# Kernel tuning notes

Measured on AMD Instinct MI355X. Metric: run time of the kernel, lower is better.

Reference implementation:

```python
import jax, jax.numpy as jnp
import numpy as np

B, S = 128, 400
EMB, ENC, DEC = 128, 1024, 300
VOCAB, MAX_OOV = 50000, 50


def setup_inputs() -> dict:
    key = jax.random.key(0)
    ks = jax.random.split(key, 16)
    s = 0.05
    return {
        "embedded": jax.random.normal(ks[0], (B, EMB), jnp.float32),
        "enc_output": jax.random.normal(ks[1], (B, S, ENC), jnp.float32),
        "h1": jax.random.normal(ks[2], (B, DEC), jnp.float32),
        "pad_mask": jnp.zeros((B, S), jnp.bool_),
        "max_n_oov": MAX_OOV,
        "source_WORD_encoding_extended": jax.random.randint(ks[3], (B, S), 0, VOCAB + MAX_OOV),
        # parameters
        "W_attn1": jax.random.normal(ks[4], (ENC, DEC), jnp.float32) * s,
        "W_attn2": jax.random.normal(ks[5], (ENC, DEC), jnp.float32) * s,
        "W_ih": jax.random.normal(ks[6], (3 * DEC, EMB + ENC), jnp.float32) * s,
        "W_hh": jax.random.normal(ks[7], (3 * DEC, DEC), jnp.float32) * s,
        "b_ih": jax.random.normal(ks[8], (3 * DEC,), jnp.float32) * s,
        "b_hh": jax.random.normal(ks[9], (3 * DEC,), jnp.float32) * s,
        "W_out": jax.random.normal(ks[10], (VOCAB, ENC + DEC), jnp.float32) * s,
        "b_out": jax.random.normal(ks[11], (VOCAB,), jnp.float32) * s,
        "W_p": jax.random.normal(ks[12], (1, ENC + DEC), jnp.float32) * s,
        "b_p": jax.random.normal(ks[13], (1,), jnp.float32) * s,
    }


def _additive_attn(h, enc_output, W, pad_mask):
    # h: [B, DEC], enc_output: [B, S, ENC], W: [ENC, DEC]
    e = jnp.einsum('bse,ed->bsd', enc_output, W)
    scores = jnp.einsum('bd,bsd->bs', h, e)
    scores = jnp.where(pad_mask, -jnp.inf, scores)
    return jax.nn.softmax(scores, axis=1)  # [B, S]


def _gru_cell(x, h, W_ih, W_hh, b_ih, b_hh):
    gx = x @ W_ih.T + b_ih  # [B, 3*DEC]
    gh = h @ W_hh.T + b_hh
    xr, xz, xn = jnp.split(gx, 3, axis=1)
    hr, hz, hn = jnp.split(gh, 3, axis=1)
    r = jax.nn.sigmoid(xr + hr)
    z = jax.nn.sigmoid(xz + hz)
    n = jnp.tanh(xn + r * hn)
    return (1.0 - z) * n + z * h


def reference(embedded, enc_output, h1, pad_mask, max_n_oov,
              source_WORD_encoding_extended, W_attn1, W_attn2,
              W_ih, W_hh, b_ih, b_hh, W_out, b_out, W_p, b_p):
    a = _additive_attn(h1, enc_output, W_attn1, pad_mask)
    weighted = jnp.einsum('bs,bse->be', a, enc_output)
    rnn_input = jnp.concatenate([embedded, weighted], axis=1)
    h_new = _gru_cell(rnn_input, h1, W_ih, W_hh, b_ih, b_hh)

    a2 = _additive_attn(h_new, enc_output, W_attn2, pad_mask)
    weighted2 = jnp.einsum('bs,bse->be', a2, enc_output)
    hw = jnp.concatenate([h_new, weighted2], axis=1)  # [B, DEC+ENC]

    p_vocab = jax.nn.softmax(hw @ W_out.T + b_out, axis=1)  # [B, VOCAB]
    p_gen = jax.nn.sigmoid(hw @ W_p.T + b_p)  # [B, 1]

    bsz = p_vocab.shape[0]
    ext_zeros = jnp.zeros((bsz, max_n_oov), p_vocab.dtype)
    p_out = p_gen * jnp.concatenate([p_vocab, ext_zeros], axis=1)
    rows = jnp.arange(bsz)[:, None]
    p_out = p_out.at[rows, source_WORD_encoding_extended].add((1.0 - p_gen) * a2)
    return p_out, h_new
```

## Files before the change

kernel.cpp:

```cpp
#include <hip/hip_runtime.h>
#include <stdint.h>

constexpr int B_     = 128;
constexpr int S_     = 400;
constexpr int EMB_   = 128;
constexpr int ENC_   = 1024;
constexpr int DEC_   = 300;
constexpr int VOCAB_ = 50000;
constexpr int OOV_   = 50;
constexpr int OUTW_  = VOCAB_ + OOV_;
constexpr int KHW_   = ENC_ + DEC_;
constexpr int KHWP_  = 1344;
constexpr int G3_    = 3 * DEC_;
constexpr int KIN_   = EMB_ + ENC_;
constexpr int CHK_   = 64;
constexpr int CHKB_  = 128;
constexpr int NC_    = 21;
constexpr int PSTRIDE_ = 1028;
constexpr int NTILE_ = 782;

typedef __attribute__((ext_vector_type(4))) float f32x4;
typedef __attribute__((ext_vector_type(8))) short short8;

__device__ __forceinline__ float dot4(float4 a, float4 b) {
  return a.x * b.x + a.y * b.y + a.z * b.z + a.w * b.w;
}

__device__ __forceinline__ short f2bf(float f) {
  uint32_t u = __builtin_bit_cast(uint32_t, f);
  u += 0x7fffu + ((u >> 16) & 1u);
  return (short)(u >> 16);
}

__global__ __launch_bounds__(256) void k_compute_v(const float* __restrict__ W,
                                                   const float* __restrict__ h,
                                                   float* __restrict__ v) {
  int b = blockIdx.x;
  __shared__ __align__(16) float hs[DEC_];
  for (int d = threadIdx.x; d < DEC_; d += 256) hs[d] = h[b * DEC_ + d];
  __syncthreads();
  for (int e = threadIdx.x; e < ENC_; e += 256) {
    const float4* w4 = (const float4*)(W + (size_t)e * DEC_);
    const float4* h4 = (const float4*)hs;
    float acc = 0.f;
    #pragma unroll 5
    for (int d = 0; d < DEC_ / 4; ++d) acc += dot4(w4[d], h4[d]);
    v[b * ENC_ + e] = acc;
  }
}

__global__ __launch_bounds__(256) void k_attn_pass(const float* __restrict__ enc,
                                                   const float* __restrict__ v,
                                                   float* __restrict__ scores,
                                                   float* __restrict__ part, int nsplit) {
  int b = blockIdx.x, split = blockIdx.y;
  int wave = threadIdx.x >> 6, lane = threadIdx.x & 63;
  float4 vr[4];
  #pragma unroll
  for (int c = 0; c < 4; ++c) vr[c] = *(const float4*)(v + b * ENC_ + c * 256 + lane * 4);
  float m = -INFINITY, l = 0.f;
  float4 wa[4];
  #pragma unroll
  for (int c = 0; c < 4; ++c) wa[c] = make_float4(0.f, 0.f, 0.f, 0.f);
  int rows = S_ / nsplit, s0 = split * rows, s_end = s0 + rows;
  int s = s0 + wave;
  for (; s + 4 < s_end; s += 8) {
    const float* era = enc + ((size_t)b * S_ + s) * ENC_;
    const float* erb = enc + ((size_t)b * S_ + s + 4) * ENC_;
    float4 e4a[4], e4b[4];
    #pragma unroll
    for (int c = 0; c < 4; ++c) {
      e4a[c] = *(const float4*)(era + c * 256 + lane * 4);
      e4b[c] = *(const float4*)(erb + c * 256 + lane * 4);
    }
    float pa = 0.f, pb = 0.f;
    #pragma unroll
    for (int c = 0; c < 4; ++c) { pa += dot4(e4a[c], vr[c]); pb += dot4(e4b[c], vr[c]); }
    #pragma unroll
    for (int off = 32; off; off >>= 1) {
      pa += __shfl_xor(pa, off);
      pb += __shfl_xor(pb, off);
    }
    if (lane == 0) { scores[b * S_ + s] = pa; scores[b * S_ + s + 4] = pb; }
    float nm = fmaxf(m, fmaxf(pa, pb));
    float sc = __expf(m - nm);
    float ea = __expf(pa - nm);
    float eb = __expf(pb - nm);
    l = l * sc + ea + eb;
    #pragma unroll
    for (int c = 0; c < 4; ++c) {
      wa[c].x = wa[c].x * sc + ea * e4a[c].x + eb * e4b[c].x;
      wa[c].y = wa[c].y * sc + ea * e4a[c].y + eb * e4b[c].y;
      wa[c].z = wa[c].z * sc + ea * e4a[c].z + eb * e4b[c].z;
      wa[c].w = wa[c].w * sc + ea * e4a[c].w + eb * e4b[c].w;
    }
    m = nm;
  }
  if (s < s_end) {
    const float* er = enc + ((size_t)b * S_ + s) * ENC_;
    float4 e4[4];
    #pragma unroll
    for (int c = 0; c < 4; ++c) e4[c] = *(const float4*)(er + c * 256 + lane * 4);
    float p = 0.f;
    #pragma unroll
    for (int c = 0; c < 4; ++c) p += dot4(e4[c], vr[c]);
    #pragma unroll
    for (int off = 32; off; off >>= 1) p += __shfl_xor(p, off);
    if (lane == 0) scores[b * S_ + s] = p;
    float nm = fmaxf(m, p);
    float sc = __expf(m - nm), pe = __expf(p - nm);
    l = l * sc + pe;
    #pragma unroll
    for (int c = 0; c < 4; ++c) {
      wa[c].x = wa[c].x * sc + pe * e4[c].x;
      wa[c].y = wa[c].y * sc + pe * e4[c].y;
      wa[c].z = wa[c].z * sc + pe * e4[c].z;
      wa[c].w = wa[c].w * sc + pe * e4[c].w;
    }
    m = nm;
  }
  float* pp = part + ((size_t)b * (nsplit * 4) + split * 4 + wave) * PSTRIDE_;
  #pragma unroll
  for (int c = 0; c < 4; ++c) *(float4*)(pp + c * 256 + lane * 4) = wa[c];
  if (lane == 0) { pp[1024] = m; pp[1025] = l; }
}

__global__ __launch_bounds__(256) void k_attn_merge1(const float* __restrict__ part, int P,
                                                     float* __restrict__ wout) {
  int b = blockIdx.x, tid = threadIdx.x;
  const float* pb = part + (size_t)b * P * PSTRIDE_;
  __shared__ float scl[64];
  __shared__ float Ls;
  if (tid < 64) {
    float mp = (tid < P) ? pb[tid * PSTRIDE_ + 1024] : -INFINITY;
    float lp = (tid < P) ? pb[tid * PSTRIDE_ + 1025] : 0.f;
    float M = mp;
    #pragma unroll
    for (int off = 32; off; off >>= 1) M = fmaxf(M, __shfl_xor(M, off));
    float e = (lp > 0.f) ? __expf(mp - M) : 0.f;
    scl[tid] = e;
    float Lc = lp * e;
    #pragma unroll
    for (int off = 32; off; off >>= 1) Lc += __shfl_xor(Lc, off);
    if (tid == 0) Ls = Lc;
  }
  __syncthreads();
  float invL = 1.f / Ls;
  for (int e = tid; e < ENC_; e += 256) {
    float acc = 0.f;
    for (int p = 0; p < P; ++p) acc += scl[p] * pb[p * PSTRIDE_ + e];
    wout[(size_t)b * ENC_ + e] = acc * invL;
  }
}

__global__ __launch_bounds__(256) void k_attn_merge2(const float* __restrict__ part, int P,
                                                     short* __restrict__ hwb,
                                                     float* __restrict__ ml,
                                                     const float* __restrict__ W_p,
                                                     const float* __restrict__ b_p,
                                                     const float* __restrict__ pg_acc,
                                                     float* __restrict__ pg) {
  int b = blockIdx.x, tid = threadIdx.x;
  const float* pb = part + (size_t)b * P * PSTRIDE_;
  __shared__ float scl[64];
  __shared__ float Ls;
  __shared__ float red[256];
  if (tid < 64) {
    float mp = (tid < P) ? pb[tid * PSTRIDE_ + 1024] : -INFINITY;
    float lp = (tid < P) ? pb[tid * PSTRIDE_ + 1025] : 0.f;
    float M = mp;
    #pragma unroll
    for (int off = 32; off; off >>= 1) M = fmaxf(M, __shfl_xor(M, off));
    float e = (lp > 0.f) ? __expf(mp - M) : 0.f;
    scl[tid] = e;
    float Lc = lp * e;
    #pragma unroll
    for (int off = 32; off; off >>= 1) Lc += __shfl_xor(Lc, off);
    if (tid == 0) { Ls = Lc; ml[b * 2] = M; ml[b * 2 + 1] = Lc; }
  }
  __syncthreads();
  float invL = 1.f / Ls;
  float pacc = 0.f;
  for (int e = tid; e < ENC_; e += 256) {
    float acc = 0.f;
    for (int p = 0; p < P; ++p) acc += scl[p] * pb[p * PSTRIDE_ + e];
    float w = acc * invL;
    hwb[(size_t)b * KHWP_ + DEC_ + e] = f2bf(w);
    pacc += w * W_p[DEC_ + e];
  }
  if (tid < KHWP_ - KHW_) hwb[(size_t)b * KHWP_ + KHW_ + tid] = 0;
  red[tid] = pacc;
  __syncthreads();
  for (int st = 128; st > 0; st >>= 1) {
    if (tid < st) red[tid] += red[tid + st];
    __syncthreads();
  }
  if (tid == 0) pg[b] = 1.f / (1.f + __expf(-(red[0] + pg_acc[b] + b_p[0])));
}

__global__ __launch_bounds__(256) void k_gates(const float* __restrict__ emb,
                                               const float* __restrict__ wgt,
                                               const float* __restrict__ h1,
                                               const float* __restrict__ W_ih,
                                               const float* __restrict__ W_hh,
                                               const float* __restrict__ b_ih,
                                               const float* __restrict__ b_hh,
                                               float* __restrict__ gx, float* __restrict__ gh,
                                               float* __restrict__ pg_acc) {
  int idx = blockIdx.x * 256 + threadIdx.x;
  if (idx < B_) pg_acc[idx] = 0.f;
  int b = idx & (B_ - 1);
  int g = idx >> 7;
  if (g >= G3_) return;
  const float4* wr = (const float4*)(W_ih + (size_t)g * KIN_);
  const float4* xe = (const float4*)(emb + b * EMB_);
  const float4* xw = (const float4*)(wgt + b * ENC_);
  float accx = b_ih[g];
  #pragma unroll 8
  for (int k = 0; k < EMB_ / 4; ++k) accx += dot4(wr[k], xe[k]);
  #pragma unroll 8
  for (int k = 0; k < ENC_ / 4; ++k) accx += dot4(wr[EMB_ / 4 + k], xw[k]);
  const float4* wh = (const float4*)(W_hh + (size_t)g * DEC_);
  const float4* xh = (const float4*)(h1 + b * DEC_);
  float acch = b_hh[g];
  #pragma unroll 5
  for (int k = 0; k < DEC_ / 4; ++k) acch += dot4(wh[k], xh[k]);
  gx[g * B_ + b] = accx;
  gh[g * B_ + b] = acch;
}

__global__ __launch_bounds__(256) void k_gru_combine(const float* __restrict__ gx,
                                                     const float* __restrict__ gh,
                                                     const float* __restrict__ h1,
                                                     float* __restrict__ hn,
                                                     short* __restrict__ hwb,
                                                     float* __restrict__ outh,
                                                     const float* __restrict__ W_p,
                                                     float* __restrict__ pg_acc) {
  int j = blockIdx.x * 256 + threadIdx.x;
  int b = blockIdx.y;
  __shared__ float red[256];
  float pp = 0.f;
  if (j < DEC_) {
    float xr = gx[j * B_ + b], xz = gx[(j + DEC_) * B_ + b], xn = gx[(j + 2 * DEC_) * B_ + b];
    float hr = gh[j * B_ + b], hz = gh[(j + DEC_) * B_ + b], hnn = gh[(j + 2 * DEC_) * B_ + b];
    float r = 1.f / (1.f + __expf(-(xr + hr)));
    float z = 1.f / (1.f + __expf(-(xz + hz)));
    float n = tanhf(xn + r * hnn);
    float h = (1.f - z) * n + z * h1[b * DEC_ + j];
    hn[b * DEC_ + j] = h;
    hwb[(size_t)b * KHWP_ + j] = f2bf(h);
    outh[b * DEC_ + j] = h;
    pp = h * W_p[j];
  }
  red[threadIdx.x] = pp;
  __syncthreads();
  for (int st = 128; st > 0; st >>= 1) {
    if (threadIdx.x < st) red[threadIdx.x] += red[threadIdx.x + st];
    __syncthreads();
  }
  if (threadIdx.x == 0) atomicAdd(pg_acc + b, red[0]);
}

__global__ __launch_bounds__(256) void k_outproj(const short* __restrict__ A,
                                                 const float* __restrict__ Wo,
                                                 const float* __restrict__ bo,
                                                 float* __restrict__ out,
                                                 float* __restrict__ pml) {
  __shared__ __align__(16) short A_lds[2 * B_ * CHK_];
  int tid = threadIdx.x;
  int wave = tid >> 6, lane = tid & 63;
  int r16 = lane & 15, kg = lane >> 4;
  int vcol = blockIdx.x * 64 + wave * 16 + r16;
  int vload = vcol < VOCAB_ ? vcol : VOCAB_ - 1;
  const float* brow = Wo + (size_t)vload * KHW_ + kg * 8;
  f32x4 acc[8];
  #pragma unroll
  for (int mi = 0; mi < 8; ++mi) acc[mi] = (f32x4){0.f, 0.f, 0.f, 0.f};

  const char* A8 = (const char*)A;
  uint32_t srcoff[4];
  #pragma unroll
  for (int i = 0; i < 4; ++i) {
    int g = tid + i * 256;
    int row = g >> 3, sp = g & 7;
    int sl = sp ^ (row & 7);
    srcoff[i] = (uint32_t)(row * 2688 + sl * 16);
  }

  float4 br[2][4];
  float  tl[8];

  #pragma unroll
  for (int i = 0; i < 4; ++i)
    __builtin_amdgcn_global_load_lds(
        (const __attribute__((address_space(1))) void*)(A8 + srcoff[i]),
        (__attribute__((address_space(3))) void*)((char*)A_lds + i * 4096 + wave * 1024),
        16, 0, 0);
  #pragma unroll
  for (int s = 0; s < 2; ++s) {
    br[0][2 * s]     = *(const float4*)(brow + s * 32);
    br[0][2 * s + 1] = *(const float4*)(brow + s * 32 + 4);
  }

  #pragma unroll
  for (int c = 0; c < NC_; ++c) {
    __syncthreads();
    if (c < NC_ - 1) {
      char* dstb = (char*)A_lds + ((c + 1) & 1) * 16384;
      #pragma unroll
      for (int i = 0; i < 4; ++i)
        __builtin_amdgcn_global_load_lds(
            (const __attribute__((address_space(1))) void*)(A8 + srcoff[i] + (c + 1) * CHKB_),
            (__attribute__((address_space(3))) void*)(dstb + i * 4096 + wave * 1024),
            16, 0, 0);
      if (c + 1 < NC_ - 1) {
        #pragma unroll
        for (int s = 0; s < 2; ++s) {
          br[(c + 1) & 1][2 * s]     = *(const float4*)(brow + (c + 1) * CHK_ + s * 32);
          br[(c + 1) & 1][2 * s + 1] = *(const float4*)(brow + (c + 1) * CHK_ + s * 32 + 4);
        }
      } else {
        br[0][0] = *(const float4*)(brow + 20 * CHK_);
        br[0][1] = *(const float4*)(brow + 20 * CHK_ + 4);
        #pragma unroll
        for (int j = 0; j < 8; ++j)
          tl[j] = (kg * 8 + j < KHW_ - 1312) ? brow[1312 + j] : 0.f;
      }
    }
    const char* rbase = (const char*)A_lds + (c & 1) * 16384 + r16 * CHKB_;
    #pragma unroll
    for (int s = 0; s < 2; ++s) {
      short8 bf;
      if (c == NC_ - 1 && s == 1) {
        #pragma unroll
        for (int j = 0; j < 8; ++j) bf[j] = f2bf(tl[j]);
      } else {
        float4 b0 = br[c & 1][2 * s], b1 = br[c & 1][2 * s + 1];
        bf[0] = f2bf(b0.x); bf[1] = f2bf(b0.y); bf[2] = f2bf(b0.z); bf[3] = f2bf(b0.w);
        bf[4] = f2bf(b1.x); bf[5] = f2bf(b1.y); bf[6] = f2bf(b1.z); bf[7] = f2bf(b1.w);
      }
      int sl = ((s << 2) + kg) ^ (r16 & 7);
      #pragma unroll
      for (int mi = 0; mi < 8; ++mi) {
        short8 af = *(const short8*)(rbase + mi * 2048 + (sl << 4));
        acc[mi] = __builtin_amdgcn_mfma_f32_16x16x32_bf16(af, bf, acc[mi], 0, 0, 0);
      }
    }
  }

  __syncthreads();
  float* wml = (float*)A_lds;

  bool valid = vcol < VOCAB_;
  float biasv = bo[vload];
  #pragma unroll
  for (int mi = 0; mi < 8; ++mi) {
    #pragma unroll
    for (int j = 0; j < 4; ++j) {
      float lv = valid ? acc[mi][j] + biasv : -INFINITY;
      if (valid) out[(size_t)(mi * 16 + kg * 4 + j) * OUTW_ + vcol] = lv;
      float mr = lv;
      #pragma unroll
      for (int msk = 1; msk < 16; msk <<= 1) mr = fmaxf(mr, __shfl_xor(mr, msk));
      float se = valid ? __expf(lv - mr) : 0.f;
      #pragma unroll
      for (int msk = 1; msk < 16; msk <<= 1) se += __shfl_xor(se, msk);
      if (r16 == 0) {
        wml[(wave * B_ + mi * 16 + kg * 4 + j) * 2]     = mr;
        wml[(wave * B_ + mi * 16 + kg * 4 + j) * 2 + 1] = se;
      }
    }
  }
  __syncthreads();
  if (tid < B_) {
    float M = -INFINITY;
    #pragma unroll
    for (int w = 0; w < 4; ++w) M = fmaxf(M, wml[(w * B_ + tid) * 2]);
    float L = 0.f;
    #pragma unroll
    for (int w = 0; w < 4; ++w) {
      float lw = wml[(w * B_ + tid) * 2 + 1];
      if (lw > 0.f) L += lw * __expf(wml[(w * B_ + tid) * 2] - M);
    }
    pml[((size_t)blockIdx.x * B_ + tid) * 2]     = M;
    pml[((size_t)blockIdx.x * B_ + tid) * 2 + 1] = L;
  }
}

__global__ __launch_bounds__(256) void k_vfinal(float* __restrict__ out,
                                                const float* __restrict__ pml,
                                                const float* __restrict__ pg,
                                                const int* __restrict__ src,
                                                const float* __restrict__ scores,
                                                const float* __restrict__ ml2) {
  int bq = blockIdx.x, b = blockIdx.y, t = threadIdx.x;
  __shared__ float rm[256], rl[256];
  float lm = -INFINITY, ll = 0.f;
  for (int tile = t; tile < NTILE_; tile += 256) {
    float m = pml[((size_t)tile * B_ + b) * 2];
    float l = pml[((size_t)tile * B_ + b) * 2 + 1];
    float M = fmaxf(lm, m);
    float nl = 0.f;
    if (ll > 0.f) nl += ll * __expf(lm - M);
    if (l > 0.f) nl += l * __expf(m - M);
    lm = M; ll = nl;
  }
  rm[t] = lm; rl[t] = ll;
  __syncthreads();
  for (int st = 128; st > 0; st >>= 1) {
    if (t < st) {
      float m1 = rm[t], l1 = rl[t], m2 = rm[t + st], l2 = rl[t + st];
      float M = fmaxf(m1, m2);
      float L = (l1 > 0.f ? l1 * __expf(m1 - M) : 0.f) + (l2 > 0.f ? l2 * __expf(m2 - M) : 0.f);
      rm[t] = M; rl[t] = L;
    }
    __syncthreads();
  }
  float M = rm[0], L = rl[0];
  float p = pg[b];
  float scale = p / L;
  float* row = out + (size_t)b * OUTW_;
  int lo = bq * 12513;
  int hi = min(lo + 12513, OUTW_);
  for (int v = lo + t; v < hi; v += 256)
    row[v] = (v < VOCAB_) ? scale * __expf(row[v] - M) : 0.f;
  __syncthreads();
  float M2 = ml2[b * 2], L2 = ml2[b * 2 + 1];
  float q = (1.f - p) / L2;
  for (int s = t; s < S_; s += 256) {
    int cidx = src[b * S_ + s];
    if (cidx >= lo && cidx < hi) {
      atomicAdd(row + cidx, q * __expf(scores[b * S_ + s] - M2));
    }
  }
}

extern "C" void kernel_launch(void* const* d_in, const int* in_sizes, int n_in,
                              void* d_out, int out_size, void* d_ws, size_t ws_size,
                              hipStream_t stream) {
  const float* embedded = (const float*)d_in[0];
  const float* enc      = (const float*)d_in[1];
  const float* h1       = (const float*)d_in[2];
  const int*   src      = (const int*)d_in[5];
  const float* W1       = (const float*)d_in[6];
  const float* W2       = (const float*)d_in[7];
  const float* W_ih     = (const float*)d_in[8];
  const float* W_hh     = (const float*)d_in[9];
  const float* b_ih     = (const float*)d_in[10];
  const float* b_hh     = (const float*)d_in[11];
  const float* W_out    = (const float*)d_in[12];
  const float* b_out    = (const float*)d_in[13];
  const float* W_p      = (const float*)d_in[14];
  const float* b_p      = (const float*)d_in[15];
  float* out = (float*)d_out;
  float* ws  = (float*)d_ws;

  size_t off = 0;
  float* v_ws    = ws + off; off += (size_t)B_ * ENC_;
  float* w1_ws   = ws + off; off += (size_t)B_ * ENC_;
  float* gx_ws   = ws + off; off += (size_t)G3_ * B_;
  float* gh_ws   = ws + off; off += (size_t)G3_ * B_;
  float* hn_ws   = ws + off; off += (size_t)B_ * DEC_;
  float* sc_ws   = ws + off; off += (size_t)B_ * S_;
  float* ml2_ws  = ws + off; off += 256;
  float* pg_ws   = ws + off; off += 128;
  float* pga_ws  = ws + off; off += 128;
  float* pml_ws  = ws + off; off += (size_t)NTILE_ * B_ * 2;
  short* hwb_ws  = (short*)(ws + off); off += (size_t)B_ * KHWP_ / 2;
  float* part_ws = ws + off;

  int NS = 16;
  while (NS > 1 && (off + (size_t)B_ * NS * 4 * PSTRIDE_) * 4 > ws_size) NS >>= 1;

  k_compute_v<<<B_, 256, 0, stream>>>(W1, h1, v_ws);
  k_attn_pass<<<dim3(B_, NS), 256, 0, stream>>>(enc, v_ws, sc_ws, part_ws, NS);
  k_attn_merge1<<<B_, 256, 0, stream>>>(part_ws, NS * 4, w1_ws);
  k_gates<<<(G3_ * B_) / 256, 256, 0, stream>>>(embedded, w1_ws, h1, W_ih, W_hh, b_ih, b_hh,
                                                gx_ws, gh_ws, pga_ws);
  k_gru_combine<<<dim3(2, B_), 256, 0, stream>>>(gx_ws, gh_ws, h1, hn_ws, hwb_ws,
                                                 out + (size_t)B_ * OUTW_, W_p, pga_ws);
  k_compute_v<<<B_, 256, 0, stream>>>(W2, hn_ws, v_ws);
  k_attn_pass<<<dim3(B_, NS), 256, 0, stream>>>(enc, v_ws, sc_ws, part_ws, NS);
  k_attn_merge2<<<B_, 256, 0, stream>>>(part_ws, NS * 4, hwb_ws, ml2_ws, W_p, b_p,
                                        pga_ws, pg_ws);
  k_outproj<<<NTILE_, 256, 0, stream>>>(hwb_ws, W_out, b_out, out, pml_ws);
  k_vfinal<<<dim3(4, B_), 256, 0, stream>>>(out, pml_ws, pg_ws, src, sc_ws, ml2_ws);
}
```

Baseline: 453.3 us.

## Fuse all phases into one persistent kernel with atomic grid barriers

Merges the ten separate kernel launches into a single persistent kernel of 768 blocks that step through the phases, separated by atomic-counter grid barriers. It also changes the attention split from up to 16 to a fixed 6 splits of 67 rows, so attention work maps onto the 768 persistent blocks. The aim is to remove launch overhead and idle tails between the small phases. The cost is spin-wait barriers, co-residency that depends on the occupancy check, fewer parallel blocks in the outproj phase (782 tiles on 768 blocks), and coarser attention parallelism.

```diff
diff --git a/kernel.cpp b/kernel.cpp
--- a/kernel.cpp
+++ b/kernel.cpp
@@ -18,6 +18,9 @@
 constexpr int NC_    = 21;
 constexpr int PSTRIDE_ = 1028;
 constexpr int NTILE_ = 782;
+constexpr int NSPL_  = 6;
+constexpr int ROWS_  = 67;
+constexpr int NBLK_  = 768;
 
 typedef __attribute__((ext_vector_type(4))) float f32x4;
 typedef __attribute__((ext_vector_type(8))) short short8;
@@ -32,14 +35,22 @@
   return (short)(u >> 16);
 }
 
-__global__ __launch_bounds__(256) void k_compute_v(const float* __restrict__ W,
-                                                   const float* __restrict__ h,
-                                                   float* __restrict__ v) {
-  int b = blockIdx.x;
-  __shared__ __align__(16) float hs[DEC_];
-  for (int d = threadIdx.x; d < DEC_; d += 256) hs[d] = h[b * DEC_ + d];
-  __syncthreads();
-  for (int e = threadIdx.x; e < ENC_; e += 256) {
+__device__ __forceinline__ void gbar(int* bar, int target) {
+  __syncthreads();
+  if (threadIdx.x == 0) {
+    __hip_atomic_fetch_add(bar, 1, __ATOMIC_RELEASE, __HIP_MEMORY_SCOPE_AGENT);
+    while (__hip_atomic_load(bar, __ATOMIC_ACQUIRE, __HIP_MEMORY_SCOPE_AGENT) < target)
+      __builtin_amdgcn_s_sleep(8);
+  }
+  __syncthreads();
+}
+
+
+__device__ void ph_compute_v(const float* __restrict__ W, const float* __restrict__ h,
+                             float* __restrict__ v, int b, int tid, float* hs) {
+  for (int d = tid; d < DEC_; d += 256) hs[d] = h[b * DEC_ + d];
+  __syncthreads();
+  for (int e = tid; e < ENC_; e += 256) {
     const float4* w4 = (const float4*)(W + (size_t)e * DEC_);
     const float4* h4 = (const float4*)hs;
     float acc = 0.f;
@@ -47,14 +58,13 @@
     for (int d = 0; d < DEC_ / 4; ++d) acc += dot4(w4[d], h4[d]);
     v[b * ENC_ + e] = acc;
   }
-}
-
-__global__ __launch_bounds__(256) void k_attn_pass(const float* __restrict__ enc,
-                                                   const float* __restrict__ v,
-                                                   float* __restrict__ scores,
-                                                   float* __restrict__ part, int nsplit) {
-  int b = blockIdx.x, split = blockIdx.y;
-  int wave = threadIdx.x >> 6, lane = threadIdx.x & 63;
+  __syncthreads();
+}
+
+__device__ void ph_attn(const float* __restrict__ enc, const float* __restrict__ v,
+                        float* __restrict__ scores, float* __restrict__ part,
+                        int b, int split, int tid) {
+  int wave = tid >> 6, lane = tid & 63;
   float4 vr[4];
   #pragma unroll
   for (int c = 0; c < 4; ++c) vr[c] = *(const float4*)(v + b * ENC_ + c * 256 + lane * 4);
@@ -62,7 +72,8 @@
   float4 wa[4];
   #pragma unroll
   for (int c = 0; c < 4; ++c) wa[c] = make_float4(0.f, 0.f, 0.f, 0.f);
-  int rows = S_ / nsplit, s0 = split * rows, s_end = s0 + rows;
+  int s0 = split * ROWS_;
+  int s_end = min(s0 + ROWS_, S_);
   int s = s0 + wave;
   for (; s + 4 < s_end; s += 8) {
     const float* era = enc + ((size_t)b * S_ + s) * ENC_;
@@ -119,18 +130,18 @@
     }
     m = nm;
   }
-  float* pp = part + ((size_t)b * (nsplit * 4) + split * 4 + wave) * PSTRIDE_;
+  float* pp = part + ((size_t)b * (NSPL_ * 4) + split * 4 + wave) * PSTRIDE_;
   #pragma unroll
   for (int c = 0; c < 4; ++c) *(float4*)(pp + c * 256 + lane * 4) = wa[c];
   if (lane == 0) { pp[1024] = m; pp[1025] = l; }
 }
 
-__global__ __launch_bounds__(256) void k_attn_merge1(const float* __restrict__ part, int P,
-                                                     float* __restrict__ wout) {
-  int b = blockIdx.x, tid = threadIdx.x;
+__device__ void ph_merge1(const float* __restrict__ part, float* __restrict__ wout,
+                          int b, int tid, float* smemf) {
+  constexpr int P = NSPL_ * 4;
   const float* pb = part + (size_t)b * P * PSTRIDE_;
-  __shared__ float scl[64];
-  __shared__ float Ls;
+  float* scl = smemf;
+  float* Lsp = smemf + 64;
   if (tid < 64) {
     float mp = (tid < P) ? pb[tid * PSTRIDE_ + 1024] : -INFINITY;
     float lp = (tid < P) ? pb[tid * PSTRIDE_ + 1025] : 0.f;
@@ -142,29 +153,27 @@
     float Lc = lp * e;
     #pragma unroll
     for (int off = 32; off; off >>= 1) Lc += __shfl_xor(Lc, off);
-    if (tid == 0) Ls = Lc;
-  }
-  __syncthreads();
-  float invL = 1.f / Ls;
+    if (tid == 0) Lsp[0] = Lc;
+  }
+  __syncthreads();
+  float invL = 1.f / Lsp[0];
   for (int e = tid; e < ENC_; e += 256) {
     float acc = 0.f;
     for (int p = 0; p < P; ++p) acc += scl[p] * pb[p * PSTRIDE_ + e];
     wout[(size_t)b * ENC_ + e] = acc * invL;
   }
-}
-
-__global__ __launch_bounds__(256) void k_attn_merge2(const float* __restrict__ part, int P,
-                                                     short* __restrict__ hwb,
-                                                     float* __restrict__ ml,
-                                                     const float* __restrict__ W_p,
-                                                     const float* __restrict__ b_p,
-                                                     const float* __restrict__ pg_acc,
-                                                     float* __restrict__ pg) {
-  int b = blockIdx.x, tid = threadIdx.x;
+  __syncthreads();
+}
+
+__device__ void ph_merge2(const float* __restrict__ part, short* __restrict__ hwb,
+                          float* __restrict__ ml, const float* __restrict__ W_p,
+                          const float* __restrict__ b_p, const float* __restrict__ pg_acc,
+                          float* __restrict__ pg, int b, int tid, float* smemf) {
+  constexpr int P = NSPL_ * 4;
   const float* pb = part + (size_t)b * P * PSTRIDE_;
-  __shared__ float scl[64];
-  __shared__ float Ls;
-  __shared__ float red[256];
+  float* scl = smemf;
+  float* Lsp = smemf + 64;
+  float* red = smemf + 80;
   if (tid < 64) {
     float mp = (tid < P) ? pb[tid * PSTRIDE_ + 1024] : -INFINITY;
     float lp = (tid < P) ? pb[tid * PSTRIDE_ + 1025] : 0.f;
@@ -176,10 +185,10 @@
     float Lc = lp * e;
     #pragma unroll
     for (int off = 32; off; off >>= 1) Lc += __shfl_xor(Lc, off);
-    if (tid == 0) { Ls = Lc; ml[b * 2] = M; ml[b * 2 + 1] = Lc; }
-  }
-  __syncthreads();
-  float invL = 1.f / Ls;
+    if (tid == 0) { Lsp[0] = Lc; ml[b * 2] = M; ml[b * 2 + 1] = Lc; }
+  }
+  __syncthreads();
+  float invL = 1.f / Lsp[0];
   float pacc = 0.f;
   for (int e = tid; e < ENC_; e += 256) {
     float acc = 0.f;
@@ -196,50 +205,44 @@
     __syncthreads();
   }
   if (tid == 0) pg[b] = 1.f / (1.f + __expf(-(red[0] + pg_acc[b] + b_p[0])));
-}
-
-__global__ __launch_bounds__(256) void k_gates(const float* __restrict__ emb,
-                                               const float* __restrict__ wgt,
-                                               const float* __restrict__ h1,
-                                               const float* __restrict__ W_ih,
-                                               const float* __restrict__ W_hh,
-                                               const float* __restrict__ b_ih,
-                                               const float* __restrict__ b_hh,
-                                               float* __restrict__ gx, float* __restrict__ gh,
-                                               float* __restrict__ pg_acc) {
-  int idx = blockIdx.x * 256 + threadIdx.x;
-  if (idx < B_) pg_acc[idx] = 0.f;
-  int b = idx & (B_ - 1);
-  int g = idx >> 7;
-  if (g >= G3_) return;
-  const float4* wr = (const float4*)(W_ih + (size_t)g * KIN_);
-  const float4* xe = (const float4*)(emb + b * EMB_);
-  const float4* xw = (const float4*)(wgt + b * ENC_);
-  float accx = b_ih[g];
-  #pragma unroll 8
-  for (int k = 0; k < EMB_ / 4; ++k) accx += dot4(wr[k], xe[k]);
-  #pragma unroll 8
-  for (int k = 0; k < ENC_ / 4; ++k) accx += dot4(wr[EMB_ / 4 + k], xw[k]);
-  const float4* wh = (const float4*)(W_hh + (size_t)g * DEC_);
-  const float4* xh = (const float4*)(h1 + b * DEC_);
-  float acch = b_hh[g];
-  #pragma unroll 5
-  for (int k = 0; k < DEC_ / 4; ++k) acch += dot4(wh[k], xh[k]);
-  gx[g * B_ + b] = accx;
-  gh[g * B_ + b] = acch;
-}
-
-__global__ __launch_bounds__(256) void k_gru_combine(const float* __restrict__ gx,
-                                                     const float* __restrict__ gh,
-                                                     const float* __restrict__ h1,
-                                                     float* __restrict__ hn,
-                                                     short* __restrict__ hwb,
-                                                     float* __restrict__ outh,
-                                                     const float* __restrict__ W_p,
-                                                     float* __restrict__ pg_acc) {
-  int j = blockIdx.x * 256 + threadIdx.x;
-  int b = blockIdx.y;
-  __shared__ float red[256];
+  __syncthreads();
+}
+
+__device__ void ph_gates(const float* __restrict__ emb, const float* __restrict__ wgt,
+                         const float* __restrict__ h1, const float* __restrict__ W_ih,
+                         const float* __restrict__ W_hh, const float* __restrict__ b_ih,
+                         const float* __restrict__ b_hh, float* __restrict__ gx,
+                         float* __restrict__ gh, float* __restrict__ pg_acc,
+                         int bid, int nblk, int tid) {
+  int idx0 = bid * 256 + tid;
+  if (idx0 < B_) pg_acc[idx0] = 0.f;
+  for (int idx = idx0; idx < G3_ * B_; idx += nblk * 256) {
+    int b = idx & (B_ - 1);
+    int g = idx >> 7;
+    const float4* wr = (const float4*)(W_ih + (size_t)g * KIN_);
+    const float4* xe = (const float4*)(emb + b * EMB_);
+    const float4* xw = (const float4*)(wgt + b * ENC_);
+    float accx = b_ih[g];
+    #pragma unroll 8
+    for (int k = 0; k < EMB_ / 4; ++k) accx += dot4(wr[k], xe[k]);
+    #pragma unroll 8
+    for (int k = 0; k < ENC_ / 4; ++k) accx += dot4(wr[EMB_ / 4 + k], xw[k]);
+    const float4* wh = (const float4*)(W_hh + (size_t)g * DEC_);
+    const float4* xh = (const float4*)(h1 + b * DEC_);
+    float acch = b_hh[g];
+    #pragma unroll 5
+    for (int k = 0; k < DEC_ / 4; ++k) acch += dot4(wh[k], xh[k]);
+    gx[g * B_ + b] = accx;
+    gh[g * B_ + b] = acch;
+  }
+}
+
+__device__ void ph_gru(const float* __restrict__ gx, const float* __restrict__ gh,
+                       const float* __restrict__ h1, float* __restrict__ hn,
+                       short* __restrict__ hwb, float* __restrict__ outh,
+                       const float* __restrict__ W_p, float* __restrict__ pg_acc,
+                       int b, int j0, int tid, float* red) {
+  int j = j0 + tid;
   float pp = 0.f;
   if (j < DEC_) {
     float xr = gx[j * B_ + b], xz = gx[(j + DEC_) * B_ + b], xn = gx[(j + 2 * DEC_) * B_ + b];
@@ -253,25 +256,24 @@
     outh[b * DEC_ + j] = h;
     pp = h * W_p[j];
   }
-  red[threadIdx.x] = pp;
+  red[tid] = pp;
   __syncthreads();
   for (int st = 128; st > 0; st >>= 1) {
-    if (threadIdx.x < st) red[threadIdx.x] += red[threadIdx.x + st];
+    if (tid < st) red[tid] += red[tid + st];
     __syncthreads();
   }
-  if (threadIdx.x == 0) atomicAdd(pg_acc + b, red[0]);
-}
-
-__global__ __launch_bounds__(256) void k_outproj(const short* __restrict__ A,
-                                                 const float* __restrict__ Wo,
-                                                 const float* __restrict__ bo,
-                                                 float* __restrict__ out,
-                                                 float* __restrict__ pml) {
-  __shared__ __align__(16) short A_lds[2 * B_ * CHK_];
-  int tid = threadIdx.x;
+  if (tid == 0) atomicAdd(pg_acc + b, red[0]);
+  __syncthreads();
+}
+
+__device__ void ph_outproj(int tile, int tid, const short* __restrict__ A,
+                           const float* __restrict__ Wo, const float* __restrict__ bo,
+                           float* __restrict__ out, float* __restrict__ pml, char* smem) {
+  __syncthreads();
+  short* A_lds = (short*)smem;
   int wave = tid >> 6, lane = tid & 63;
   int r16 = lane & 15, kg = lane >> 4;
-  int vcol = blockIdx.x * 64 + wave * 16 + r16;
+  int vcol = tile * 64 + wave * 16 + r16;
   int vload = vcol < VOCAB_ ? vcol : VOCAB_ - 1;
   const float* brow = Wo + (size_t)vload * KHW_ + kg * 8;
   f32x4 acc[8];
@@ -383,21 +385,19 @@
       float lw = wml[(w * B_ + tid) * 2 + 1];
       if (lw > 0.f) L += lw * __expf(wml[(w * B_ + tid) * 2] - M);
     }
-    pml[((size_t)blockIdx.x * B_ + tid) * 2]     = M;
-    pml[((size_t)blockIdx.x * B_ + tid) * 2 + 1] = L;
-  }
-}
-
-__global__ __launch_bounds__(256) void k_vfinal(float* __restrict__ out,
-                                                const float* __restrict__ pml,
-                                                const float* __restrict__ pg,
-                                                const int* __restrict__ src,
-                                                const float* __restrict__ scores,
-                                                const float* __restrict__ ml2) {
-  int bq = blockIdx.x, b = blockIdx.y, t = threadIdx.x;
-  __shared__ float rm[256], rl[256];
+    pml[((size_t)tile * B_ + tid) * 2]     = M;
+    pml[((size_t)tile * B_ + tid) * 2 + 1] = L;
+  }
+}
+
+__device__ void ph_vfinal(int bq, int b, int tid, float* __restrict__ out,
+                          const float* __restrict__ pml, const float* __restrict__ pg,
+                          const int* __restrict__ src, const float* __restrict__ scores,
+                          const float* __restrict__ ml2, float* smemf) {
+  float* rm = smemf;
+  float* rl = smemf + 256;
   float lm = -INFINITY, ll = 0.f;
-  for (int tile = t; tile < NTILE_; tile += 256) {
+  for (int tile = tid; tile < NTILE_; tile += 256) {
     float m = pml[((size_t)tile * B_ + b) * 2];
     float l = pml[((size_t)tile * B_ + b) * 2 + 1];
     float M = fmaxf(lm, m);
@@ -406,14 +406,14 @@
     if (l > 0.f) nl += l * __expf(m - M);
     lm = M; ll = nl;
   }
-  rm[t] = lm; rl[t] = ll;
+  rm[tid] = lm; rl[tid] = ll;
   __syncthreads();
   for (int st = 128; st > 0; st >>= 1) {
-    if (t < st) {
-      float m1 = rm[t], l1 = rl[t], m2 = rm[t + st], l2 = rl[t + st];
+    if (tid < st) {
+      float m1 = rm[tid], l1 = rl[tid], m2 = rm[tid + st], l2 = rl[tid + st];
       float M = fmaxf(m1, m2);
       float L = (l1 > 0.f ? l1 * __expf(m1 - M) : 0.f) + (l2 > 0.f ? l2 * __expf(m2 - M) : 0.f);
-      rm[t] = M; rl[t] = L;
+      rm[tid] = M; rl[tid] = L;
     }
     __syncthreads();
   }
@@ -423,17 +423,98 @@
   float* row = out + (size_t)b * OUTW_;
   int lo = bq * 12513;
   int hi = min(lo + 12513, OUTW_);
-  for (int v = lo + t; v < hi; v += 256)
+  for (int v = lo + tid; v < hi; v += 256)
     row[v] = (v < VOCAB_) ? scale * __expf(row[v] - M) : 0.f;
   __syncthreads();
   float M2 = ml2[b * 2], L2 = ml2[b * 2 + 1];
   float q = (1.f - p) / L2;
-  for (int s = t; s < S_; s += 256) {
+  for (int s = tid; s < S_; s += 256) {
     int cidx = src[b * S_ + s];
-    if (cidx >= lo && cidx < hi) {
+    if (cidx >= lo && cidx < hi)
       atomicAdd(row + cidx, q * __expf(scores[b * S_ + s] - M2));
-    }
-  }
+  }
+}
+
+
+__global__ __launch_bounds__(256) void k_mega(
+    const float* embedded, const float* enc, const float* h1, const int* src,
+    const float* W1, const float* W2, const float* W_ih, const float* W_hh,
+    const float* b_ih, const float* b_hh, const float* W_out, const float* b_out,
+    const float* W_p, const float* b_p, float* out,
+    float* v_ws, float* w1_ws, float* gx_ws, float* gh_ws, float* hn_ws,
+    float* sc_ws, float* ml2_ws, float* pg_ws, float* pga_ws, float* pml_ws,
+    short* hwb_ws, float* part_ws, int* bar) {
+  __shared__ __align__(16) char smem[2 * B_ * CHK_ * 2];
+  int bid = blockIdx.x, tid = threadIdx.x;
+  if (bid < B_) ph_compute_v(W1, h1, v_ws, bid, tid, (float*)smem);
+  gbar(bar, 1 * NBLK_);
+  ph_attn(enc, v_ws, sc_ws, part_ws, bid / NSPL_, bid % NSPL_, tid);
+  gbar(bar, 2 * NBLK_);
+  if (bid < B_) ph_merge1(part_ws, w1_ws, bid, tid, (float*)smem);
+  gbar(bar, 3 * NBLK_);
+  ph_gates(embedded, w1_ws, h1, W_ih, W_hh, b_ih, b_hh, gx_ws, gh_ws, pga_ws, bid, NBLK_, tid);
+  gbar(bar, 4 * NBLK_);
+  if (bid < 2 * B_)
+    ph_gru(gx_ws, gh_ws, h1, hn_ws, hwb_ws, out + (size_t)B_ * OUTW_, W_p, pga_ws,
+           bid >> 1, (bid & 1) * 256, tid, (float*)smem);
+  gbar(bar, 5 * NBLK_);
+  if (bid < B_) ph_compute_v(W2, hn_ws, v_ws, bid, tid, (float*)smem);
+  gbar(bar, 6 * NBLK_);
+  ph_attn(enc, v_ws, sc_ws, part_ws, bid / NSPL_, bid % NSPL_, tid);
+  gbar(bar, 7 * NBLK_);
+  if (bid < B_) ph_merge2(part_ws, hwb_ws, ml2_ws, W_p, b_p, pga_ws, pg_ws, bid, tid, (float*)smem);
+  gbar(bar, 8 * NBLK_);
+  for (int t = bid; t < NTILE_; t += NBLK_)
+    ph_outproj(t, tid, hwb_ws, W_out, b_out, out, pml_ws, smem);
+  gbar(bar, 9 * NBLK_);
+  if (bid < 4 * B_)
+    ph_vfinal(bid & 3, bid >> 2, tid, out, pml_ws, pg_ws, src, sc_ws, ml2_ws, (float*)smem);
+}
+
+
+__global__ __launch_bounds__(256) void k_compute_v(const float* W, const float* h, float* v) {
+  __shared__ __align__(16) float hs[DEC_];
+  ph_compute_v(W, h, v, blockIdx.x, threadIdx.x, hs);
+}
+__global__ __launch_bounds__(256) void k_attn_pass(const float* enc, const float* v,
+                                                   float* scores, float* part) {
+  ph_attn(enc, v, scores, part, blockIdx.x, blockIdx.y, threadIdx.x);
+}
+__global__ __launch_bounds__(256) void k_attn_merge1(const float* part, float* wout) {
+  __shared__ __align__(16) float sm[80];
+  ph_merge1(part, wout, blockIdx.x, threadIdx.x, sm);
+}
+__global__ __launch_bounds__(256) void k_attn_merge2(const float* part, short* hwb, float* ml,
+                                                     const float* W_p, const float* b_p,
+                                                     const float* pga, float* pg) {
+  __shared__ __align__(16) float sm[336];
+  ph_merge2(part, hwb, ml, W_p, b_p, pga, pg, blockIdx.x, threadIdx.x, sm);
+}
+__global__ __launch_bounds__(256) void k_gates(const float* emb, const float* wgt,
+                                               const float* h1, const float* W_ih,
+                                               const float* W_hh, const float* b_ih,
+                                               const float* b_hh, float* gx, float* gh,
+                                               float* pga) {
+  ph_gates(emb, wgt, h1, W_ih, W_hh, b_ih, b_hh, gx, gh, pga, blockIdx.x, gridDim.x,
+           threadIdx.x);
+}
+__global__ __launch_bounds__(256) void k_gru_combine(const float* gx, const float* gh,
+                                                     const float* h1, float* hn, short* hwb,
+                                                     float* outh, const float* W_p,
+                                                     float* pga) {
+  __shared__ __align__(16) float red[256];
+  ph_gru(gx, gh, h1, hn, hwb, outh, W_p, pga, blockIdx.y, blockIdx.x * 256, threadIdx.x, red);
+}
+__global__ __launch_bounds__(256) void k_outproj(const short* A, const float* Wo,
+                                                 const float* bo, float* out, float* pml) {
+  __shared__ __align__(16) char smem[2 * B_ * CHK_ * 2];
+  ph_outproj(blockIdx.x, threadIdx.x, A, Wo, bo, out, pml, smem);
+}
+__global__ __launch_bounds__(256) void k_vfinal(float* out, const float* pml, const float* pg,
+                                                const int* src, const float* scores,
+                                                const float* ml2) {
+  __shared__ __align__(16) float sm[512];
+  ph_vfinal(blockIdx.x, blockIdx.y, threadIdx.x, out, pml, pg, src, scores, ml2, sm);
 }
 
 extern "C" void kernel_launch(void* const* d_in, const int* in_sizes, int n_in,
@@ -466,24 +547,33 @@
   float* ml2_ws  = ws + off; off += 256;
   float* pg_ws   = ws + off; off += 128;
   float* pga_ws  = ws + off; off += 128;
+  int*   bar_ws  = (int*)(ws + off); off += 64;
   float* pml_ws  = ws + off; off += (size_t)NTILE_ * B_ * 2;
   short* hwb_ws  = (short*)(ws + off); off += (size_t)B_ * KHWP_ / 2;
   float* part_ws = ws + off;
 
-  int NS = 16;
-  while (NS > 1 && (off + (size_t)B_ * NS * 4 * PSTRIDE_) * 4 > ws_size) NS >>= 1;
-
-  k_compute_v<<<B_, 256, 0, stream>>>(W1, h1, v_ws);
-  k_attn_pass<<<dim3(B_, NS), 256, 0, stream>>>(enc, v_ws, sc_ws, part_ws, NS);
-  k_attn_merge1<<<B_, 256, 0, stream>>>(part_ws, NS * 4, w1_ws);
-  k_gates<<<(G3_ * B_) / 256, 256, 0, stream>>>(embedded, w1_ws, h1, W_ih, W_hh, b_ih, b_hh,
-                                                gx_ws, gh_ws, pga_ws);
-  k_gru_combine<<<dim3(2, B_), 256, 0, stream>>>(gx_ws, gh_ws, h1, hn_ws, hwb_ws,
-                                                 out + (size_t)B_ * OUTW_, W_p, pga_ws);
-  k_compute_v<<<B_, 256, 0, stream>>>(W2, hn_ws, v_ws);
-  k_attn_pass<<<dim3(B_, NS), 256, 0, stream>>>(enc, v_ws, sc_ws, part_ws, NS);
-  k_attn_merge2<<<B_, 256, 0, stream>>>(part_ws, NS * 4, hwb_ws, ml2_ws, W_p, b_p,
-                                        pga_ws, pg_ws);
-  k_outproj<<<NTILE_, 256, 0, stream>>>(hwb_ws, W_out, b_out, out, pml_ws);
-  k_vfinal<<<dim3(4, B_), 256, 0, stream>>>(out, pml_ws, pg_ws, src, sc_ws, ml2_ws);
-}
+  hipMemsetAsync(bar_ws, 0, 256, stream);
+
+  int occ = 0;
+  hipOccupancyMaxActiveBlocksPerMultiprocessor(&occ, (const void*)k_mega, 256, 0);
+
+  if (occ >= 3) {
+    k_mega<<<NBLK_, 256, 0, stream>>>(
+        embedded, enc, h1, src, W1, W2, W_ih, W_hh, b_ih, b_hh, W_out, b_out,
+        W_p, b_p, out, v_ws, w1_ws, gx_ws, gh_ws, hn_ws, sc_ws, ml2_ws, pg_ws,
+        pga_ws, pml_ws, hwb_ws, part_ws, bar_ws);
+  } else {
+    k_compute_v<<<B_, 256, 0, stream>>>(W1, h1, v_ws);
+    k_attn_pass<<<dim3(B_, NSPL_), 256, 0, stream>>>(enc, v_ws, sc_ws, part_ws);
+    k_attn_merge1<<<B_, 256, 0, stream>>>(part_ws, w1_ws);
+    k_gates<<<(G3_ * B_) / 256, 256, 0, stream>>>(embedded, w1_ws, h1, W_ih, W_hh, b_ih,
+                                                  b_hh, gx_ws, gh_ws, pga_ws);
+    k_gru_combine<<<dim3(2, B_), 256, 0, stream>>>(gx_ws, gh_ws, h1, hn_ws, hwb_ws,
+                                                   out + (size_t)B_ * OUTW_, W_p, pga_ws);
+    k_compute_v<<<B_, 256, 0, stream>>>(W2, hn_ws, v_ws);
+    k_attn_pass<<<dim3(B_, NSPL_), 256, 0, stream>>>(enc, v_ws, sc_ws, part_ws);
+    k_attn_merge2<<<B_, 256, 0, stream>>>(part_ws, hwb_ws, ml2_ws, W_p, b_p, pga_ws, pg_ws);
+    k_outproj<<<NTILE_, 256, 0, stream>>>(hwb_ws, W_out, b_out, out, pml_ws);
+    k_vfinal<<<dim3(4, B_), 256, 0, stream>>>(out, pml_ws, pg_ws, src, sc_ws, ml2_ws);
+  }
+}
```

Result: faster. 432.2 us (-4.7%).
